# Kernel tuning notes

Measured on AMD Instinct MI355X. Metric: run time of the kernel, lower is better.

The kernel has to match this reference:

```python
import jax, jax.numpy as jnp
import numpy as np

N_NODES = 65536
N_EDGES = 1048576
IN_DIM = 512
HID = 128


def gcn_conv(x, W, b, src, dst, ew, n_nodes):
    """PyG GCNConv: h = D^{-1/2} (A + I) D^{-1/2} (x W) + b, with edge weights."""
    h = x @ W  # [N, out]
    # add self-loops with weight 1
    loop = jnp.arange(n_nodes, dtype=src.dtype)
    src_f = jnp.concatenate([src, loop])
    dst_f = jnp.concatenate([dst, loop])
    ew_f = jnp.concatenate([ew, jnp.ones((n_nodes,), dtype=h.dtype)])
    # symmetric normalization: deg computed on destination (in-degree)
    deg = jax.ops.segment_sum(ew_f, dst_f, num_segments=n_nodes)
    dinv = jnp.where(deg > 0, jax.lax.rsqrt(deg), 0.0).astype(h.dtype)
    norm = dinv[src_f] * ew_f * dinv[dst_f]  # [E+N]
    msgs = norm[:, None] * h[src_f]  # gather + scale
    out = jax.ops.segment_sum(msgs, dst_f, num_segments=n_nodes)
    return out + b


def setup_inputs() -> dict:
    key = jax.random.key(0)
    ks = jax.random.split(key, 7)
    x = jax.random.normal(ks[0], (N_NODES, IN_DIM), dtype=jnp.float32)
    edge_index = jax.random.randint(ks[1], (2, N_EDGES), 0, N_NODES, dtype=jnp.int64 if jax.config.jax_enable_x64 else jnp.int32)
    edge_weight = jax.random.uniform(ks[2], (N_EDGES,), dtype=jnp.float32)
    s1 = 1.0 / np.sqrt(IN_DIM)
    s2 = 1.0 / np.sqrt(HID)
    W1 = jax.random.uniform(ks[3], (IN_DIM, HID), minval=-s1, maxval=s1, dtype=jnp.float32)
    b1 = jnp.zeros((HID,), dtype=jnp.float32)
    W2 = jax.random.uniform(ks[4], (HID, HID), minval=-s2, maxval=s2, dtype=jnp.float32)
    b2 = jnp.zeros((HID,), dtype=jnp.float32)
    return {"x": x, "edge_index": edge_index, "edge_weight": edge_weight,
            "W1": W1, "b1": b1, "W2": W2, "b2": b2}


def reference(x, edge_index, edge_weight, W1, b1, W2, b2):
    src, dst = edge_index[0], edge_index[1]
    h = gcn_conv(x, W1, b1, src, dst, edge_weight, N_NODES)
    h = jax.nn.relu(h)
    # dropout is identity at inference (training=False)
    z = gcn_conv(h, W2, b2, src, dst, edge_weight, N_NODES)
    return z
```

## Files before the change

kernel.cpp:

```cpp
#include <hip/hip_runtime.h>

#define NN 65536
#define NE 1048576
#define INDIM 512
#define HID 128
#define NSB 256

typedef __attribute__((ext_vector_type(8))) short bf16x8;
typedef __attribute__((ext_vector_type(16))) float f32x16;

__global__ void k_h1(const int* __restrict__ dst, int* __restrict__ ghist) {
    __shared__ int hcnt[256];
    hcnt[threadIdx.x] = 0;
    __syncthreads();
    int base = blockIdx.x * 4096;
#pragma unroll
    for (int r = 0; r < 16; r++)
        atomicAdd(&hcnt[dst[base + r * 256 + threadIdx.x] & 255], 1);
    __syncthreads();
    ghist[threadIdx.x * NSB + blockIdx.x] = hcnt[threadIdx.x];
}

__global__ void k_scan_ex(int* data, int* bsum, int n) {
    __shared__ int tmp[256];
    int i = blockIdx.x * 256 + threadIdx.x;
    int v = (i < n) ? data[i] : 0;
    tmp[threadIdx.x] = v;
    __syncthreads();
    for (int off = 1; off < 256; off <<= 1) {
        int t = (threadIdx.x >= off) ? tmp[threadIdx.x - off] : 0;
        __syncthreads();
        tmp[threadIdx.x] += t;
        __syncthreads();
    }
    if (i < n) data[i] = tmp[threadIdx.x] - v;
    if (threadIdx.x == 255 && bsum) bsum[blockIdx.x] = tmp[255];
}

__global__ void k_addback(int* data, const int* __restrict__ bsum) {
    int i = blockIdx.x * 256 + threadIdx.x;
    data[i] += bsum[blockIdx.x];
}

__global__ void k_s1(const int* __restrict__ src, const int* __restrict__ dst,
                     const float* __restrict__ ew, const int* __restrict__ ghist,
                     unsigned* __restrict__ e1sd, float* __restrict__ e1ew) {
    __shared__ int cur[256];
    cur[threadIdx.x] = ghist[threadIdx.x * NSB + blockIdx.x];
    __syncthreads();
    int base = blockIdx.x * 4096;
#pragma unroll
    for (int r = 0; r < 16; r++) {
        int e = base + r * 256 + threadIdx.x;
        int d = dst[e];
        int p = atomicAdd(&cur[d & 255], 1);
        e1sd[p] = (unsigned)src[e] | ((unsigned)(d >> 8) << 16);
        e1ew[p] = ew[e];
    }
}

__global__ void k_s2(const int* __restrict__ ghist, const unsigned* __restrict__ e1sd,
                     const float* __restrict__ e1ew,
                     uint2* __restrict__ edata, int* __restrict__ row_beg,
                     int* __restrict__ row_end, float* __restrict__ dinv) {
    __shared__ int cnt[256];
    __shared__ float degs[256];
    __shared__ int tmp[256];
    __shared__ int curx[256];
    const int bin = blockIdx.x;
    const int t = threadIdx.x;
    cnt[t] = 0;
    degs[t] = 0.f;
    __syncthreads();
    const int binstart = ghist[bin * NSB];
    const int binend = (bin == 255) ? NE : ghist[(bin + 1) * NSB];
    for (int i = binstart + t; i < binend; i += 256) {
        unsigned u = e1sd[i];
        int j = u >> 16;
        atomicAdd(&cnt[j], 1);
        atomicAdd(&degs[j], e1ew[i]);
    }
    __syncthreads();
    int v = cnt[t];
    tmp[t] = v;
    __syncthreads();
    for (int off = 1; off < 256; off <<= 1) {
        int u = (t >= off) ? tmp[t - off] : 0;
        __syncthreads();
        tmp[t] += u;
        __syncthreads();
    }
    int offt = tmp[t] - v;
    int d = (t << 8) | bin;
    int beg = binstart + offt;
    row_beg[d] = beg;
    row_end[d] = beg + v;
    dinv[d] = rsqrtf(1.0f + degs[t]);
    curx[t] = beg;
    __syncthreads();
    for (int i = binstart + t; i < binend; i += 256) {
        unsigned u = e1sd[i];
        int p = atomicAdd(&curx[u >> 16], 1);
        edata[p] = make_uint2(u & 0xFFFFu, __float_as_uint(e1ew[i]));
    }
}

template <int K>
__global__ void k_prep_pack(const float* __restrict__ W, unsigned short* __restrict__ P) {
    int t = blockIdx.x * 256 + threadIdx.x;
    int l = t & 63;
    int h = (t >> 6) & 1;
    int n = (t >> 7) & 3;
    int k0 = t >> 9;
    if (k0 >= K / 16) return;
    int colg = n * 32 + (l & 31);
    int kbase = k0 * 16 + (l >> 5) * 8;
    bf16x8 v;
#pragma unroll
    for (int j = 0; j < 8; j++) {
        float f = W[(size_t)(kbase + j) * 128 + colg];
        unsigned b = __float_as_uint(f);
        if (h == 0) {
            v[j] = (short)(b >> 16);
        } else {
            float lf = f - __uint_as_float(b & 0xFFFF0000u);
            v[j] = (short)(__float_as_uint(lf) >> 16);
        }
    }
    *(bf16x8*)(P + (size_t)t * 8) = v;
}

__device__ __forceinline__ void split8(const float4& a0, const float4& a1,
                                       bf16x8& hi, bf16x8& lo) {
    float f[8] = {a0.x, a0.y, a0.z, a0.w, a1.x, a1.y, a1.z, a1.w};
#pragma unroll
    for (int i = 0; i < 8; i++) {
        unsigned b = __float_as_uint(f[i]);
        unsigned hb = b & 0xFFFF0000u;
        float lf = f[i] - __uint_as_float(hb);
        hi[i] = (short)(hb >> 16);
        lo[i] = (short)(__float_as_uint(lf) >> 16);
    }
}

__device__ __forceinline__ unsigned short f2bf_rne(float v) {
    unsigned u = __float_as_uint(v);
    unsigned r = (u + 0x7FFFu + ((u >> 16) & 1u)) >> 16;
    return (unsigned short)r;
}

template <int K>
__device__ __forceinline__ void stage_chunk(const float* __restrict__ A, int rowbase,
                                            const unsigned short* __restrict__ Bp,
                                            int c, int tid, float* As, unsigned short* Bs) {
    const int w = tid >> 6;
#pragma unroll
    for (int q = 0; q < 2; ++q) {
        int lh = (tid >> 7) & 1;
        int row = (tid >> 1) & 63;
        int g = (tid & 1) ^ ((row >> 2) & 1);
        const float* src = A + (size_t)(rowbase + row) * K + c * 32 + q * 16 + lh * 8 + g * 4;
        char* dst = (char*)As + (size_t)(q * 256 + w * 64) * 16;
        __builtin_amdgcn_global_load_lds((const __attribute__((address_space(1))) void*)src,
                                         (__attribute__((address_space(3))) void*)dst, 16, 0, 0);
    }
    const char* bsrc0 = (const char*)Bp + (size_t)c * 16384;
#pragma unroll
    for (int q = 0; q < 4; ++q) {
        const char* src = bsrc0 + (size_t)(q * 256 + tid) * 16;
        char* dst = (char*)Bs + (size_t)(q * 256 + w * 64) * 16;
        __builtin_amdgcn_global_load_lds((const __attribute__((address_space(1))) void*)src,
                                         (__attribute__((address_space(3))) void*)dst, 16, 0, 0);
    }
}

template <int K>
__global__ __launch_bounds__(256, 2) void k_gemm_mfma(const float* __restrict__ A,
                                                      const unsigned short* __restrict__ Bp,
                                                      unsigned short* __restrict__ Cb) {
    constexpr int NC = K / 32;
    __shared__ __align__(16) float As[3][2048];
    __shared__ __align__(16) unsigned short Bs[3][8192];
    const int tid = threadIdx.x;
    const int w = tid >> 6;
    const int lane = tid & 63;
    const int l31 = lane & 31;
    const int lhalf = lane >> 5;
    const int rowbase = blockIdx.x * 64;
    const int ncol = (w & 1) * 2;
    const int r = (w >> 1) * 32 + l31;
    const int xr = (l31 >> 2) & 1;

    f32x16 acc[2] = {};

    stage_chunk<K>(A, rowbase, Bp, 0, tid, As[0], Bs[0]);
    stage_chunk<K>(A, rowbase, Bp, 1, tid, As[1], Bs[1]);

    for (int c = 0; c < NC; ++c) {
        if (c > 0) {
            __builtin_amdgcn_s_barrier();
            asm volatile("" ::: "memory");
            __builtin_amdgcn_sched_barrier(0);
        }
        if (c + 2 < NC) {
            int b = (c + 2) % 3;
            stage_chunk<K>(A, rowbase, Bp, c + 2, tid, As[b], Bs[b]);
        }
        int rem = NC - 1 - c;
        if (rem >= 2)      asm volatile("s_waitcnt vmcnt(12)" ::: "memory");
        else if (rem == 1) asm volatile("s_waitcnt vmcnt(6)" ::: "memory");
        else               asm volatile("s_waitcnt vmcnt(0)" ::: "memory");
        __builtin_amdgcn_s_barrier();
        const int cur = c % 3;
#pragma unroll
        for (int kk = 0; kk < 2; ++kk) {
            int bg = ((kk * 2 + lhalf) * 64 + r) * 2;
            float4 aa = *(const float4*)&As[cur][(size_t)(bg + xr) * 4];
            float4 ab = *(const float4*)&As[cur][(size_t)(bg + (1 ^ xr)) * 4];
            bf16x8 ahi, alo;
            split8(aa, ab, ahi, alo);
#pragma unroll
            for (int n = 0; n < 2; ++n) {
                int f = (ncol + n) * 2;
                bf16x8 bhi = *(const bf16x8*)&Bs[cur][(size_t)((kk * 8 + f) * 64 + lane) * 8];
                bf16x8 blo = *(const bf16x8*)&Bs[cur][(size_t)((kk * 8 + f + 1) * 64 + lane) * 8];
                acc[n] = __builtin_amdgcn_mfma_f32_32x32x16_bf16(ahi, bhi, acc[n], 0, 0, 0);
                acc[n] = __builtin_amdgcn_mfma_f32_32x32x16_bf16(ahi, blo, acc[n], 0, 0, 0);
                acc[n] = __builtin_amdgcn_mfma_f32_32x32x16_bf16(alo, bhi, acc[n], 0, 0, 0);
            }
        }
    }

    const int rbase = rowbase + (w >> 1) * 32 + 4 * lhalf;
#pragma unroll
    for (int n = 0; n < 2; ++n) {
        const int col = (ncol + n) * 32 + l31;
#pragma unroll
        for (int rr = 0; rr < 16; ++rr) {
            int rout = rbase + (rr & 3) + 8 * (rr >> 2);
            Cb[(size_t)rout * HID + col] = f2bf_rne(acc[n][rr]);
        }
    }
}

__device__ __forceinline__ float2 up2(unsigned u) {
    float2 r;
    r.x = __uint_as_float(u << 16);
    r.y = __uint_as_float(u & 0xFFFF0000u);
    return r;
}

template <bool RELU>
__global__ __launch_bounds__(256) void k_agg(const unsigned short* __restrict__ hb,
                                             const float* __restrict__ dinv,
                                             const int* __restrict__ row_beg,
                                             const int* __restrict__ row_end,
                                             const uint2* __restrict__ edata,
                                             const float* __restrict__ bias,
                                             float* __restrict__ out) {
    int d = (blockIdx.x * blockDim.x + threadIdx.x) >> 6;
    int lane = threadIdx.x & 63;
    float di = dinv[d];
    float2 hv = up2(((const unsigned*)(hb + (size_t)d * HID))[lane]);
    int beg = row_beg[d], end = row_end[d];
    float ex = 0.f, ey = 0.f;
    int e = beg;
    for (; e + 15 < end; e += 16) {
        uint2 u[16];
        unsigned g[16];
        float dv[16];
#pragma unroll
        for (int q = 0; q < 16; q++) u[q] = edata[e + q];
#pragma unroll
        for (int q = 0; q < 16; q++) {
            g[q] = ((const unsigned*)(hb + (size_t)u[q].x * HID))[lane];
            dv[q] = dinv[u[q].x];
        }
#pragma unroll
        for (int q = 0; q < 16; q++) {
            float2 vv = up2(g[q]);
            float c = dv[q] * __uint_as_float(u[q].y);
            ex += c * vv.x;
            ey += c * vv.y;
        }
    }
    for (; e + 3 < end; e += 4) {
        uint2 u[4];
        unsigned g[4];
        float dv[4];
#pragma unroll
        for (int q = 0; q < 4; q++) u[q] = edata[e + q];
#pragma unroll
        for (int q = 0; q < 4; q++) {
            g[q] = ((const unsigned*)(hb + (size_t)u[q].x * HID))[lane];
            dv[q] = dinv[u[q].x];
        }
#pragma unroll
        for (int q = 0; q < 4; q++) {
            float2 vv = up2(g[q]);
            float c = dv[q] * __uint_as_float(u[q].y);
            ex += c * vv.x;
            ey += c * vv.y;
        }
    }
    for (; e < end; ++e) {
        uint2 u = edata[e];
        float2 v = up2(((const unsigned*)(hb + (size_t)u.x * HID))[lane]);
        float c = dinv[u.x] * __uint_as_float(u.y);
        ex += c * v.x;
        ey += c * v.y;
    }
    float2 bv = ((const float2*)bias)[lane];
    float selfc = di * di;
    float ax = di * ex + selfc * hv.x + bv.x;
    float ay = di * ey + selfc * hv.y + bv.y;
    if (RELU) {
        ax = fmaxf(ax, 0.f);
        ay = fmaxf(ay, 0.f);
    }
    float2 rr;
    rr.x = ax;
    rr.y = ay;
    ((float2*)(out + (size_t)d * HID))[lane] = rr;
}

extern "C" void kernel_launch(void* const* d_in, const int* in_sizes, int n_in,
                              void* d_out, int out_size, void* d_ws, size_t ws_size,
                              hipStream_t stream) {
    const float* x = (const float*)d_in[0];
    const int* ei = (const int*)d_in[1];
    const float* ew = (const float*)d_in[2];
    const float* W1 = (const float*)d_in[3];
    const float* b1 = (const float*)d_in[4];
    const float* W2 = (const float*)d_in[5];
    const float* b2 = (const float*)d_in[6];
    const int* src = ei;
    const int* dst = ei + NE;
    float* out = (float*)d_out;

    char* ws = (char*)d_ws;
    unsigned short* hb = (unsigned short*)(ws + 0);
    uint2* edata    = (uint2*)(ws + 16777216);
    int*   ghist    = (int*)(ws + 25165824);
    int*   bsum1    = (int*)(ws + 25427968);
    unsigned* e1sd  = (unsigned*)(ws + 25428992);
    float* e1ew     = (float*)(ws + 29623296);
    int*   row_beg  = (int*)(ws + 33817600);
    int*   row_end  = (int*)(ws + 34079744);
    float* dinv     = (float*)(ws + 34341888);
    unsigned short* bp1 = (unsigned short*)(ws + 34604032);
    unsigned short* bp2 = (unsigned short*)(ws + 34866176);

    k_h1<<<NSB, 256, 0, stream>>>(dst, ghist);
    k_scan_ex<<<NSB, 256, 0, stream>>>(ghist, bsum1, 256 * NSB);
    k_scan_ex<<<1, 256, 0, stream>>>(bsum1, nullptr, NSB);
    k_addback<<<NSB, 256, 0, stream>>>(ghist, bsum1);
    k_s1<<<NSB, 256, 0, stream>>>(src, dst, ew, ghist, e1sd, e1ew);
    k_s2<<<256, 256, 0, stream>>>(ghist, e1sd, e1ew, edata, row_beg, row_end, dinv);
    k_prep_pack<INDIM><<<(INDIM / 16) * 8 * 64 / 256, 256, 0, stream>>>(W1, bp1);
    k_prep_pack<HID><<<(HID / 16) * 8 * 64 / 256, 256, 0, stream>>>(W2, bp2);

    k_gemm_mfma<INDIM><<<NN / 64, 256, 0, stream>>>(x, bp1, hb);
    k_agg<true><<<NN / 4, 256, 0, stream>>>(hb, dinv, row_beg, row_end, edata, b1, out);

    k_gemm_mfma<HID><<<NN / 64, 256, 0, stream>>>(out, bp2, hb);
    k_agg<false><<<NN / 4, 256, 0, stream>>>(hb, dinv, row_beg, row_end, edata, b2, out);
}
```

Before: 202.7 us.

## Emit pre-split bf16 hi/lo activations from layer-1 aggregation for second GEMM

The first aggregation kernel now writes its ReLU output directly as packed bf16 hi and lo halves instead of fp32. The second GEMM gets a PRESPLIT path that loads these halves straight into LDS, so it no longer converts and splits fp32 in its inner loop. The two weight-pack kernels are merged into one launch. Traffic for the intermediate stays the same (two bf16 halves equal one fp32). The main saving is the split ALU work in the GEMM plus one kernel launch. The gain depends on how expensive that split work is relative to the loads.

```diff
diff --git a/kernel.cpp b/kernel.cpp
--- a/kernel.cpp
+++ b/kernel.cpp
@@ -105,14 +105,12 @@
     }
 }
 
-template <int K>
-__global__ void k_prep_pack(const float* __restrict__ W, unsigned short* __restrict__ P) {
-    int t = blockIdx.x * 256 + threadIdx.x;
+__device__ __forceinline__ void prep_one(const float* __restrict__ W, unsigned short* __restrict__ P,
+                                         int t) {
     int l = t & 63;
     int h = (t >> 6) & 1;
     int n = (t >> 7) & 3;
     int k0 = t >> 9;
-    if (k0 >= K / 16) return;
     int colg = n * 32 + (l & 31);
     int kbase = k0 * 16 + (l >> 5) * 8;
     bf16x8 v;
@@ -130,6 +128,13 @@
     *(bf16x8*)(P + (size_t)t * 8) = v;
 }
 
+__global__ void k_prep_pack2(const float* __restrict__ W1, unsigned short* __restrict__ P1,
+                             const float* __restrict__ W2, unsigned short* __restrict__ P2) {
+    int t = blockIdx.x * 256 + threadIdx.x;
+    if (t < 16384) prep_one(W1, P1, t);
+    else if (t < 16384 + 4096) prep_one(W2, P2, t - 16384);
+}
+
 __device__ __forceinline__ void split8(const float4& a0, const float4& a1,
                                        bf16x8& hi, bf16x8& lo) {
     float f[8] = {a0.x, a0.y, a0.z, a0.w, a1.x, a1.y, a1.z, a1.w};
@@ -149,37 +154,61 @@
     return (unsigned short)r;
 }
 
-template <int K>
-__device__ __forceinline__ void stage_chunk(const float* __restrict__ A, int rowbase,
+template <int K, bool PRESPLIT>
+__device__ __forceinline__ void stage_chunk(const float* __restrict__ A,
+                                            const unsigned short* __restrict__ Ahi,
+                                            const unsigned short* __restrict__ Alo,
+                                            int rowbase,
                                             const unsigned short* __restrict__ Bp,
-                                            int c, int tid, float* As, unsigned short* Bs) {
+                                            int c, int tid, char* As, unsigned short* Bs) {
     const int w = tid >> 6;
-#pragma unroll
-    for (int q = 0; q < 2; ++q) {
-        int lh = (tid >> 7) & 1;
-        int row = (tid >> 1) & 63;
-        int g = (tid & 1) ^ ((row >> 2) & 1);
-        const float* src = A + (size_t)(rowbase + row) * K + c * 32 + q * 16 + lh * 8 + g * 4;
-        char* dst = (char*)As + (size_t)(q * 256 + w * 64) * 16;
-        __builtin_amdgcn_global_load_lds((const __attribute__((address_space(1))) void*)src,
+    if (PRESPLIT) {
+        {
+            int row = tid & 63;
+            int kk2lh = tid >> 6;
+            const char* srcp = (const char*)Ahi + ((size_t)(rowbase + row) * 128 + c * 32 + kk2lh * 8) * 2;
+            char* dst = As + (size_t)(w * 64) * 16;
+            __builtin_amdgcn_global_load_lds((const __attribute__((address_space(1))) void*)srcp,
+                                             (__attribute__((address_space(3))) void*)dst, 16, 0, 0);
+        }
+        {
+            int row = tid & 63;
+            int kk2lh = tid >> 6;
+            const char* srcp = (const char*)Alo + ((size_t)(rowbase + row) * 128 + c * 32 + kk2lh * 8) * 2;
+            char* dst = As + 4096 + (size_t)(w * 64) * 16;
+            __builtin_amdgcn_global_load_lds((const __attribute__((address_space(1))) void*)srcp,
+                                             (__attribute__((address_space(3))) void*)dst, 16, 0, 0);
+        }
+    } else {
+#pragma unroll
+        for (int q = 0; q < 2; ++q) {
+            int lh = (tid >> 7) & 1;
+            int row = (tid >> 1) & 63;
+            int g = (tid & 1) ^ ((row >> 2) & 1);
+            const float* srcp = A + (size_t)(rowbase + row) * K + c * 32 + q * 16 + lh * 8 + g * 4;
+            char* dst = As + (size_t)(q * 256 + w * 64) * 16;
+            __builtin_amdgcn_global_load_lds((const __attribute__((address_space(1))) void*)srcp,
+                                             (__attribute__((address_space(3))) void*)dst, 16, 0, 0);
+        }
+    }
+    const char* bsrc0 = (const char*)Bp + (size_t)c * 16384;
+#pragma unroll
+    for (int q = 0; q < 4; ++q) {
+        const char* srcp = bsrc0 + (size_t)(q * 256 + tid) * 16;
+        char* dst = (char*)Bs + (size_t)(q * 256 + w * 64) * 16;
+        __builtin_amdgcn_global_load_lds((const __attribute__((address_space(1))) void*)srcp,
                                          (__attribute__((address_space(3))) void*)dst, 16, 0, 0);
     }
-    const char* bsrc0 = (const char*)Bp + (size_t)c * 16384;
-#pragma unroll
-    for (int q = 0; q < 4; ++q) {
-        const char* src = bsrc0 + (size_t)(q * 256 + tid) * 16;
-        char* dst = (char*)Bs + (size_t)(q * 256 + w * 64) * 16;
-        __builtin_amdgcn_global_load_lds((const __attribute__((address_space(1))) void*)src,
-                                         (__attribute__((address_space(3))) void*)dst, 16, 0, 0);
-    }
-}
-
-template <int K>
+}
+
+template <int K, bool PRESPLIT>
 __global__ __launch_bounds__(256, 2) void k_gemm_mfma(const float* __restrict__ A,
+                                                      const unsigned short* __restrict__ Ahi,
+                                                      const unsigned short* __restrict__ Alo,
                                                       const unsigned short* __restrict__ Bp,
                                                       unsigned short* __restrict__ Cb) {
     constexpr int NC = K / 32;
-    __shared__ __align__(16) float As[3][2048];
+    __shared__ __align__(16) char As[3][8192];
     __shared__ __align__(16) unsigned short Bs[3][8192];
     const int tid = threadIdx.x;
     const int w = tid >> 6;
@@ -193,8 +222,8 @@
 
     f32x16 acc[2] = {};
 
-    stage_chunk<K>(A, rowbase, Bp, 0, tid, As[0], Bs[0]);
-    stage_chunk<K>(A, rowbase, Bp, 1, tid, As[1], Bs[1]);
+    stage_chunk<K, PRESPLIT>(A, Ahi, Alo, rowbase, Bp, 0, tid, As[0], Bs[0]);
+    stage_chunk<K, PRESPLIT>(A, Ahi, Alo, rowbase, Bp, 1, tid, As[1], Bs[1]);
 
     for (int c = 0; c < NC; ++c) {
         if (c > 0) {
@@ -204,7 +233,7 @@
         }
         if (c + 2 < NC) {
             int b = (c + 2) % 3;
-            stage_chunk<K>(A, rowbase, Bp, c + 2, tid, As[b], Bs[b]);
+            stage_chunk<K, PRESPLIT>(A, Ahi, Alo, rowbase, Bp, c + 2, tid, As[b], Bs[b]);
         }
         int rem = NC - 1 - c;
         if (rem >= 2)      asm volatile("s_waitcnt vmcnt(12)" ::: "memory");
@@ -214,11 +243,18 @@
         const int cur = c % 3;
 #pragma unroll
         for (int kk = 0; kk < 2; ++kk) {
-            int bg = ((kk * 2 + lhalf) * 64 + r) * 2;
-            float4 aa = *(const float4*)&As[cur][(size_t)(bg + xr) * 4];
-            float4 ab = *(const float4*)&As[cur][(size_t)(bg + (1 ^ xr)) * 4];
             bf16x8 ahi, alo;
-            split8(aa, ab, ahi, alo);
+            if (PRESPLIT) {
+                int gidx = ((kk * 2 + lhalf) * 64 + r) * 16;
+                ahi = *(const bf16x8*)&As[cur][gidx];
+                alo = *(const bf16x8*)&As[cur][4096 + gidx];
+            } else {
+                const float* Af = (const float*)As[cur];
+                int bg = ((kk * 2 + lhalf) * 64 + r) * 2;
+                float4 aa = *(const float4*)&Af[(size_t)(bg + xr) * 4];
+                float4 ab = *(const float4*)&Af[(size_t)(bg + (1 ^ xr)) * 4];
+                split8(aa, ab, ahi, alo);
+            }
 #pragma unroll
             for (int n = 0; n < 2; ++n) {
                 int f = (ncol + n) * 2;
@@ -257,7 +293,9 @@
                                              const int* __restrict__ row_end,
                                              const uint2* __restrict__ edata,
                                              const float* __restrict__ bias,
-                                             float* __restrict__ out) {
+                                             float* __restrict__ out,
+                                             unsigned* __restrict__ a1hi,
+                                             unsigned* __restrict__ a1lo) {
     int d = (blockIdx.x * blockDim.x + threadIdx.x) >> 6;
     int lane = threadIdx.x & 63;
     float di = dinv[d];
@@ -317,11 +355,18 @@
     if (RELU) {
         ax = fmaxf(ax, 0.f);
         ay = fmaxf(ay, 0.f);
-    }
-    float2 rr;
-    rr.x = ax;
-    rr.y = ay;
-    ((float2*)(out + (size_t)d * HID))[lane] = rr;
+        unsigned bx = __float_as_uint(ax), by = __float_as_uint(ay);
+        unsigned hx = bx & 0xFFFF0000u, hy = by & 0xFFFF0000u;
+        unsigned lx = __float_as_uint(ax - __uint_as_float(hx));
+        unsigned ly = __float_as_uint(ay - __uint_as_float(hy));
+        a1hi[(size_t)d * 64 + lane] = (hx >> 16) | (hy & 0xFFFF0000u);
+        a1lo[(size_t)d * 64 + lane] = (lx >> 16) | (ly & 0xFFFF0000u);
+    } else {
+        float2 rr;
+        rr.x = ax;
+        rr.y = ay;
+        ((float2*)(out + (size_t)d * HID))[lane] = rr;
+    }
 }
 
 extern "C" void kernel_launch(void* const* d_in, const int* in_sizes, int n_in,
@@ -350,6 +395,8 @@
     float* dinv     = (float*)(ws + 34341888);
     unsigned short* bp1 = (unsigned short*)(ws + 34604032);
     unsigned short* bp2 = (unsigned short*)(ws + 34866176);
+    unsigned* a1hi  = (unsigned*)(ws + 35651584);
+    unsigned* a1lo  = (unsigned*)(ws + 52428800);
 
     k_h1<<<NSB, 256, 0, stream>>>(dst, ghist);
     k_scan_ex<<<NSB, 256, 0, stream>>>(ghist, bsum1, 256 * NSB);
@@ -357,12 +404,12 @@
     k_addback<<<NSB, 256, 0, stream>>>(ghist, bsum1);
     k_s1<<<NSB, 256, 0, stream>>>(src, dst, ew, ghist, e1sd, e1ew);
     k_s2<<<256, 256, 0, stream>>>(ghist, e1sd, e1ew, edata, row_beg, row_end, dinv);
-    k_prep_pack<INDIM><<<(INDIM / 16) * 8 * 64 / 256, 256, 0, stream>>>(W1, bp1);
-    k_prep_pack<HID><<<(HID / 16) * 8 * 64 / 256, 256, 0, stream>>>(W2, bp2);
-
-    k_gemm_mfma<INDIM><<<NN / 64, 256, 0, stream>>>(x, bp1, hb);
-    k_agg<true><<<NN / 4, 256, 0, stream>>>(hb, dinv, row_beg, row_end, edata, b1, out);
-
-    k_gemm_mfma<HID><<<NN / 64, 256, 0, stream>>>(out, bp2, hb);
-    k_agg<false><<<NN / 4, 256, 0, stream>>>(hb, dinv, row_beg, row_end, edata, b2, out);
-}
+    k_prep_pack2<<<80, 256, 0, stream>>>(W1, bp1, W2, bp2);
+
+    k_gemm_mfma<INDIM, false><<<NN / 64, 256, 0, stream>>>(x, nullptr, nullptr, bp1, hb);
+    k_agg<true><<<NN / 4, 256, 0, stream>>>(hb, dinv, row_beg, row_end, edata, b1, nullptr, a1hi, a1lo);
+
+    k_gemm_mfma<HID, true><<<NN / 64, 256, 0, stream>>>(nullptr, (const unsigned short*)a1hi,
+                                                        (const unsigned short*)a1lo, bp2, hb);
+    k_agg<false><<<NN / 4, 256, 0, stream>>>(hb, dinv, row_beg, row_end, edata, b2, out, nullptr, nullptr);
+}
```

Result: no change. 203.5 us (+0.4%).
